# Performance work log

Measured on AMD Instinct MI355X. Metric: run time of the kernel, lower is better.

The kernel has to match this reference:

```python
import jax, jax.numpy as jnp
import numpy as np

BLOCK = 32


def _dct_constants(bs):
    # Replicates get_dct_constants + the sorting/reshaping done in DCTEncoderLayer.__init__
    x, y = np.meshgrid(np.arange(bs), np.arange(bs), indexing='xy')
    basis = np.zeros((bs, bs, bs, bs), dtype=np.float32)
    mag = np.zeros((bs, bs), dtype=np.float64)
    fac = np.zeros((bs, bs), dtype=np.float32)
    for v in range(bs):
        for u in range(bs):
            xb = np.cos((2 * x + 1) * u * np.pi / (2 * bs))
            yb = np.cos((2 * y + 1) * v * np.pi / (2 * bs))
            basis[v, u] = (xb * yb).astype(np.float32)
            mag[v, u] = np.linalg.norm(np.array([v, u], dtype=np.int64))
            c_v = 1 / np.sqrt(2) if v == 0 else 1.0
            c_u = 1 / np.sqrt(2) if u == 0 else 1.0
            fac[v, u] = c_u * c_v
    kernels = basis.reshape(-1, bs, bs)
    factors = fac.reshape(-1)
    idx = np.argsort(mag.reshape(-1))  # same default argsort as the torch module
    return kernels[idx].astype(np.float32), factors[idx].astype(np.float32)


def setup_inputs() -> dict:
    key = jax.random.key(0)
    rgb = jax.random.uniform(key, (32, 3, 512, 512), dtype=jnp.float32)
    kernels, factors = _dct_constants(BLOCK)
    return {
        "rgb_images_batch": rgb,
        "kernels": jnp.asarray(kernels),   # [K=bs^2, bs, bs], sorted by freq magnitude
        "factors": jnp.asarray(factors),   # [K]
    }


def _rgb_to_ycbcr(rgb):
    # kornia.color.rgb_to_ycbcr (delta = 0.5)
    r, g, b = rgb[:, 0], rgb[:, 1], rgb[:, 2]
    y = 0.299 * r + 0.587 * g + 0.114 * b
    cb = (b - y) * 0.564 + 0.5
    cr = (r - y) * 0.713 + 0.5
    return jnp.stack([y, cb, cr], axis=1)  # [B,3,H,W]


def reference(rgb_images_batch, kernels, factors):
    bs = BLOCK
    B, C, H, W = rgb_images_batch.shape
    nh, nw = H // bs, W // bs
    ycbcr = 2.0 * _rgb_to_ycbcr(rgb_images_batch) - 1.0            # [B,3,H,W]
    # non-overlapping blocks: [B,3,nh,nw,bs,bs]
    blocks = ycbcr.reshape(B, 3, nh, bs, nw, bs).transpose(0, 1, 2, 4, 3, 5)
    # stride=bs conv2d with dense DCT basis kernels == per-block contraction
    coeffs = jnp.einsum('bcmnxy,kxy->bckmn', blocks, kernels)      # [B,3,K,nh,nw]
    scale = (2.0 / bs) * factors                                   # [K]
    coeffs = coeffs * scale[None, None, :, None, None]
    # torch.cat([y, cb, cr], dim=1) -> [B, 3*K, nh, nw]
    return coeffs.reshape(B, 3 * bs * bs, nh, nw)
```

## Files before the change

kernel.cpp:

```cpp
#include <hip/hip_runtime.h>
#include <math.h>


typedef __bf16 bf16x8 __attribute__((ext_vector_type(8)));
typedef float  f32x4  __attribute__((ext_vector_type(4)));

#define PI_F 3.14159265358979323846f

__device__ __forceinline__ unsigned short f2bf(float f) {
    union { float f; unsigned u; } v; v.f = f;
    unsigned u = v.u;
    u += 0x7fffu + ((u >> 16) & 1u);
    return (unsigned short)(u >> 16);
}

__global__ __launch_bounds__(256) void setup_kernel(const float* __restrict__ kern,
                                                    const float* __restrict__ factors,
                                                    unsigned short* __restrict__ Cbf,
                                                    int2* __restrict__ T2) {
    int k = blockIdx.x * 256 + threadIdx.x;
    int i = k & 31, t = k >> 5;
    Cbf[k] = f2bf(cosf((float)((2 * i + 1) * t) * (PI_F / 64.f)));

    float k00 = kern[(size_t)k * 1024];
    float rv  = kern[(size_t)k * 1024 + 32] / k00;
    float ru  = kern[(size_t)k * 1024 + 1]  / k00;
    float cv2 = fminf(fmaxf((rv + 3.f) * 0.25f, 0.f), 1.f);
    float cu2 = fminf(fmaxf((ru + 3.f) * 0.25f, 0.f), 1.f);
    int v = __float2int_rn(acosf(sqrtf(cv2)) * (64.f / PI_F));
    int u = __float2int_rn(acosf(sqrtf(cu2)) * (64.f / PI_F));
    float s = factors[k] * (2.f / 32.f);
    int vq = (v >> 2) & 3, vh = v >> 4, vr = v & 3;
    T2[(u * 4 + vq) * 8 + vh * 4 + vr] = make_int2(k, __float_as_int(s));
}

__global__ __launch_bounds__(512, 6) void dct_fused(const float* __restrict__ rgb,
                                                    const unsigned short* __restrict__ Cbf,
                                                    const int2* __restrict__ T2,
                                                    float* __restrict__ out) {
    __shared__ __align__(16) unsigned char Tls[32 * 1280];

    const int tid  = threadIdx.x;
    const int lane = tid & 63;
    const int w    = tid >> 6;
    const int quad = lane >> 4;
    const int l15  = lane & 15;
    const int g    = blockIdx.x;
    const int bc   = g >> 4;
    const int b    = bc / 3;
    const int c    = bc - b * 3;
    const int loc  = g & 15;
    const int m    = ((loc & 7) << 1) | (loc >> 3);

    float ar, ag, ab, ao;
    if (c == 0)      { ar =  0.598f;     ag =  1.174f;     ab =  0.228f;     ao = -1.f; }
    else if (c == 1) { ar = -0.337272f;  ag = -0.662136f;  ab =  0.999408f;  ao =  0.f; }
    else             { ar =  0.999626f;  ag = -0.837062f;  ab = -0.162564f;  ao =  0.f; }

    const float* prow = rgb + (size_t)b * 786432
                            + (size_t)(m * 32 + w * 4) * 512
                            + (size_t)l15 * 32 + (size_t)quad * 8;
    f32x4 acc[4][2];
    {
        float4 buf[4][2];
#pragma unroll
        for (int xi = 0; xi < 4; ++xi) {
            buf[xi][0] = *(const float4*)(prow + (size_t)xi * 512);
            buf[xi][1] = *(const float4*)(prow + (size_t)xi * 512 + 4);
        }
#pragma unroll
        for (int xi = 0; xi < 4; ++xi)
            for (int h = 0; h < 2; ++h) {
                acc[xi][h][0] = ar * buf[xi][h].x;
                acc[xi][h][1] = ar * buf[xi][h].y;
                acc[xi][h][2] = ar * buf[xi][h].z;
                acc[xi][h][3] = ar * buf[xi][h].w;
            }
#pragma unroll
        for (int xi = 0; xi < 4; ++xi) {
            buf[xi][0] = *(const float4*)(prow + 262144 + (size_t)xi * 512);
            buf[xi][1] = *(const float4*)(prow + 262144 + (size_t)xi * 512 + 4);
        }
#pragma unroll
        for (int xi = 0; xi < 4; ++xi)
            for (int h = 0; h < 2; ++h) {
                acc[xi][h][0] += ag * buf[xi][h].x;
                acc[xi][h][1] += ag * buf[xi][h].y;
                acc[xi][h][2] += ag * buf[xi][h].z;
                acc[xi][h][3] += ag * buf[xi][h].w;
            }
#pragma unroll
        for (int xi = 0; xi < 4; ++xi) {
            buf[xi][0] = *(const float4*)(prow + 524288 + (size_t)xi * 512);
            buf[xi][1] = *(const float4*)(prow + 524288 + (size_t)xi * 512 + 4);
        }
#pragma unroll
        for (int xi = 0; xi < 4; ++xi)
            for (int h = 0; h < 2; ++h) {
                acc[xi][h][0] += ab * buf[xi][h].x;
                acc[xi][h][1] += ab * buf[xi][h].y;
                acc[xi][h][2] += ab * buf[xi][h].z;
                acc[xi][h][3] += ab * buf[xi][h].w;
            }
    }
    bf16x8 fr[4];
#pragma unroll
    for (int xi = 0; xi < 4; ++xi) {
        union { bf16x8 v; unsigned short s[8]; } f;
#pragma unroll
        for (int e = 0; e < 8; ++e)
            f.s[e] = f2bf(acc[xi][e >> 2][e & 3] + ao);
        fr[xi] = f.v;
    }

    union { bf16x8 v; unsigned short s[8]; } af0, af1;
    af0.v = *(const bf16x8*)(Cbf + l15 * 32 + quad * 8);
    af1.v = *(const bf16x8*)(Cbf + (16 + l15) * 32 + quad * 8);

    const f32x4 zero = {0.f, 0.f, 0.f, 0.f};

#pragma unroll
    for (int fh = 0; fh < 2; ++fh) {
        f32x4 dd[4];
#pragma unroll
        for (int xi = 0; xi < 4; ++xi)
            dd[xi] = __builtin_amdgcn_mfma_f32_16x16x32_bf16(
                fh ? af1.v : af0.v, fr[xi], zero, 0, 0, 0);
#pragma unroll
        for (int r = 0; r < 4; ++r) {
            const int f1 = fh * 16 + quad * 4 + r;
            ushort4 pk;
            pk.x = f2bf(dd[0][r]);
            pk.y = f2bf(dd[1][r]);
            pk.z = f2bf(dd[2][r]);
            pk.w = f2bf(dd[3][r]);
            *(ushort4*)(Tls + f1 * 1280 + l15 * 80 + w * 8) = pk;
        }
    }
    __syncthreads();

    const size_t obase = (size_t)bc * 262144 + (size_t)m * 16 + (size_t)l15;
#pragma unroll
    for (int i = 0; i < 4; ++i) {
        const int f1 = w * 4 + i;
        union { int4 q[4]; int2 e[8]; } tt;
        const int4* tp = (const int4*)(T2 + ((f1 * 4 + quad) << 3));
        tt.q[0] = tp[0]; tt.q[1] = tp[1]; tt.q[2] = tp[2]; tt.q[3] = tp[3];
        bf16x8 bfr = *(const bf16x8*)(Tls + f1 * 1280 + l15 * 80 + quad * 16);
#pragma unroll
        for (int uh = 0; uh < 2; ++uh) {
            f32x4 d2 = __builtin_amdgcn_mfma_f32_16x16x32_bf16(
                uh ? af1.v : af0.v, bfr, zero, 0, 0, 0);
#pragma unroll
            for (int r = 0; r < 4; ++r) {
                int2 ks = tt.e[uh * 4 + r];
                out[obase + (size_t)ks.x * 256] = d2[r] * __int_as_float(ks.y);
            }
        }
    }
}

extern "C" void kernel_launch(void* const* d_in, const int* in_sizes, int n_in,
                              void* d_out, int out_size, void* d_ws, size_t ws_size,
                              hipStream_t stream) {
    const float* rgb     = (const float*)d_in[0];
    const float* kern    = (const float*)d_in[1];
    const float* factors = (const float*)d_in[2];
    float* out = (float*)d_out;

    unsigned short* Cbf = (unsigned short*)d_ws;
    int2* T2 = (int2*)((char*)d_ws + 8192);

    setup_kernel<<<4, 256, 0, stream>>>(kern, factors, Cbf, T2);
    dct_fused<<<1536, 512, 0, stream>>>(rgb, Cbf, T2, out);
}
```

Baseline: 210.4 us.

## Double-buffer RGB plane loads, hoist constant loads, and stage T2 table in LDS

Issues loads of the first two color planes up front into separate register buffers, with asm barriers that keep them live so more global loads are in flight per wave. The Cbf fragment loads and the T2 index table load are moved to kernel start, and T2 is staged into shared memory so the epilogue reads it from LDS instead of global memory. Occupancy hint drops from 6 to 4 blocks per CU to allow the extra registers, which reduces latency hiding through concurrent waves.

```diff
diff --git a/kernel.cpp b/kernel.cpp
--- a/kernel.cpp
+++ b/kernel.cpp
@@ -6,6 +6,9 @@
 typedef float  f32x4  __attribute__((ext_vector_type(4)));
 
 #define PI_F 3.14159265358979323846f
+
+#define KEEP8(B) asm volatile("" : "+v"(B[0]), "+v"(B[1]), "+v"(B[2]), "+v"(B[3]), \
+                                   "+v"(B[4]), "+v"(B[5]), "+v"(B[6]), "+v"(B[7]))
 
 __device__ __forceinline__ unsigned short f2bf(float f) {
     union { float f; unsigned u; } v; v.f = f;
@@ -34,11 +37,12 @@
     T2[(u * 4 + vq) * 8 + vh * 4 + vr] = make_int2(k, __float_as_int(s));
 }
 
-__global__ __launch_bounds__(512, 6) void dct_fused(const float* __restrict__ rgb,
+__global__ __launch_bounds__(512, 4) void dct_fused(const float* __restrict__ rgb,
                                                     const unsigned short* __restrict__ Cbf,
                                                     const int2* __restrict__ T2,
                                                     float* __restrict__ out) {
     __shared__ __align__(16) unsigned char Tls[32 * 1280];
+    __shared__ __align__(16) unsigned char T2ls[8192];
 
     const int tid  = threadIdx.x;
     const int lane = tid & 63;
@@ -52,6 +56,12 @@
     const int loc  = g & 15;
     const int m    = ((loc & 7) << 1) | (loc >> 3);
 
+    int4 t2chunk = *((const int4*)T2 + tid);
+
+    union { bf16x8 v; unsigned short s[8]; } af0, af1;
+    af0.v = *(const bf16x8*)(Cbf + l15 * 32 + quad * 8);
+    af1.v = *(const bf16x8*)(Cbf + (16 + l15) * 32 + quad * 8);
+
     float ar, ag, ab, ao;
     if (c == 0)      { ar =  0.598f;     ag =  1.174f;     ab =  0.228f;     ao = -1.f; }
     else if (c == 1) { ar = -0.337272f;  ag = -0.662136f;  ab =  0.999408f;  ao =  0.f; }
@@ -60,49 +70,57 @@
     const float* prow = rgb + (size_t)b * 786432
                             + (size_t)(m * 32 + w * 4) * 512
                             + (size_t)l15 * 32 + (size_t)quad * 8;
+    f32x4 bufA[8], bufB[8];
     f32x4 acc[4][2];
-    {
-        float4 buf[4][2];
+
 #pragma unroll
-        for (int xi = 0; xi < 4; ++xi) {
-            buf[xi][0] = *(const float4*)(prow + (size_t)xi * 512);
-            buf[xi][1] = *(const float4*)(prow + (size_t)xi * 512 + 4);
+    for (int xi = 0; xi < 4; ++xi) {
+        bufA[2 * xi]     = *(const f32x4*)(prow + (size_t)xi * 512);
+        bufA[2 * xi + 1] = *(const f32x4*)(prow + (size_t)xi * 512 + 4);
+    }
+#pragma unroll
+    for (int xi = 0; xi < 4; ++xi) {
+        bufB[2 * xi]     = *(const f32x4*)(prow + 262144 + (size_t)xi * 512);
+        bufB[2 * xi + 1] = *(const f32x4*)(prow + 262144 + (size_t)xi * 512 + 4);
+    }
+    *(int4*)(T2ls + tid * 16) = t2chunk;
+
+    KEEP8(bufA);
+#pragma unroll
+    for (int xi = 0; xi < 4; ++xi)
+#pragma unroll
+        for (int h = 0; h < 2; ++h) {
+            acc[xi][h][0] = ar * bufA[2 * xi + h][0];
+            acc[xi][h][1] = ar * bufA[2 * xi + h][1];
+            acc[xi][h][2] = ar * bufA[2 * xi + h][2];
+            acc[xi][h][3] = ar * bufA[2 * xi + h][3];
         }
 #pragma unroll
-        for (int xi = 0; xi < 4; ++xi)
-            for (int h = 0; h < 2; ++h) {
-                acc[xi][h][0] = ar * buf[xi][h].x;
-                acc[xi][h][1] = ar * buf[xi][h].y;
-                acc[xi][h][2] = ar * buf[xi][h].z;
-                acc[xi][h][3] = ar * buf[xi][h].w;
-            }
+    for (int xi = 0; xi < 4; ++xi) {
+        bufA[2 * xi]     = *(const f32x4*)(prow + 524288 + (size_t)xi * 512);
+        bufA[2 * xi + 1] = *(const f32x4*)(prow + 524288 + (size_t)xi * 512 + 4);
+    }
+    KEEP8(bufB);
 #pragma unroll
-        for (int xi = 0; xi < 4; ++xi) {
-            buf[xi][0] = *(const float4*)(prow + 262144 + (size_t)xi * 512);
-            buf[xi][1] = *(const float4*)(prow + 262144 + (size_t)xi * 512 + 4);
+    for (int xi = 0; xi < 4; ++xi)
+#pragma unroll
+        for (int h = 0; h < 2; ++h) {
+            acc[xi][h][0] += ag * bufB[2 * xi + h][0];
+            acc[xi][h][1] += ag * bufB[2 * xi + h][1];
+            acc[xi][h][2] += ag * bufB[2 * xi + h][2];
+            acc[xi][h][3] += ag * bufB[2 * xi + h][3];
         }
+    KEEP8(bufA);
 #pragma unroll
-        for (int xi = 0; xi < 4; ++xi)
-            for (int h = 0; h < 2; ++h) {
-                acc[xi][h][0] += ag * buf[xi][h].x;
-                acc[xi][h][1] += ag * buf[xi][h].y;
-                acc[xi][h][2] += ag * buf[xi][h].z;
-                acc[xi][h][3] += ag * buf[xi][h].w;
-            }
+    for (int xi = 0; xi < 4; ++xi)
 #pragma unroll
-        for (int xi = 0; xi < 4; ++xi) {
-            buf[xi][0] = *(const float4*)(prow + 524288 + (size_t)xi * 512);
-            buf[xi][1] = *(const float4*)(prow + 524288 + (size_t)xi * 512 + 4);
+        for (int h = 0; h < 2; ++h) {
+            acc[xi][h][0] += ab * bufA[2 * xi + h][0];
+            acc[xi][h][1] += ab * bufA[2 * xi + h][1];
+            acc[xi][h][2] += ab * bufA[2 * xi + h][2];
+            acc[xi][h][3] += ab * bufA[2 * xi + h][3];
         }
-#pragma unroll
-        for (int xi = 0; xi < 4; ++xi)
-            for (int h = 0; h < 2; ++h) {
-                acc[xi][h][0] += ab * buf[xi][h].x;
-                acc[xi][h][1] += ab * buf[xi][h].y;
-                acc[xi][h][2] += ab * buf[xi][h].z;
-                acc[xi][h][3] += ab * buf[xi][h].w;
-            }
-    }
+
     bf16x8 fr[4];
 #pragma unroll
     for (int xi = 0; xi < 4; ++xi) {
@@ -112,10 +130,6 @@
             f.s[e] = f2bf(acc[xi][e >> 2][e & 3] + ao);
         fr[xi] = f.v;
     }
-
-    union { bf16x8 v; unsigned short s[8]; } af0, af1;
-    af0.v = *(const bf16x8*)(Cbf + l15 * 32 + quad * 8);
-    af1.v = *(const bf16x8*)(Cbf + (16 + l15) * 32 + quad * 8);
 
     const f32x4 zero = {0.f, 0.f, 0.f, 0.f};
 
@@ -144,8 +158,11 @@
     for (int i = 0; i < 4; ++i) {
         const int f1 = w * 4 + i;
         union { int4 q[4]; int2 e[8]; } tt;
-        const int4* tp = (const int4*)(T2 + ((f1 * 4 + quad) << 3));
-        tt.q[0] = tp[0]; tt.q[1] = tp[1]; tt.q[2] = tp[2]; tt.q[3] = tp[3];
+        const unsigned char* tp = T2ls + (f1 * 4 + quad) * 64;
+        tt.q[0] = *(const int4*)(tp);
+        tt.q[1] = *(const int4*)(tp + 16);
+        tt.q[2] = *(const int4*)(tp + 32);
+        tt.q[3] = *(const int4*)(tp + 48);
         bf16x8 bfr = *(const bf16x8*)(Tls + f1 * 1280 + l15 * 80 + quad * 16);
 #pragma unroll
         for (int uh = 0; uh < 2; ++uh) {
```

Result: faster. 204.4 us (-2.8%).
